# Performance work log

Hardware: AMD Instinct MI355X
Metric: run time of the kernel (lower is better)

The kernel has to match this reference:

```python
import jax, jax.numpy as jnp
import numpy as np

TOP_K = 2


def setup_inputs() -> dict:
    key = jax.random.key(0)
    k1, k2, k3, k4 = jax.random.split(key, 4)
    B, S, H, I, E = 2, 1024, 2048, 1408, 8
    hidden_states = jax.random.normal(k1, (B, S, H), dtype=jnp.float32)
    gate_w = jax.random.normal(k2, (E, H), dtype=jnp.float32) * (1.0 / np.sqrt(H))
    # stacked expert weights: gate_up_proj [E, 2I, H], down_proj [E, H, I] (torch Linear [out,in])
    w1 = jax.random.normal(k3, (E, 2 * I, H), dtype=jnp.float32) * (1.0 / np.sqrt(H))
    w2 = jax.random.normal(k4, (E, H, I), dtype=jnp.float32) * (1.0 / np.sqrt(I))
    return {"hidden_states": hidden_states, "gate_w": gate_w, "w1": w1, "w2": w2}


def reference(hidden_states, gate_w, w1, w2):
    B, S, H = hidden_states.shape
    E = gate_w.shape[0]
    T = B * S
    x = hidden_states.reshape(T, H)

    # --- gating: softmax -> top-k -> renormalize ---
    logits = jnp.einsum('th,eh->te', x, gate_w)            # [T, E]
    probs = jax.nn.softmax(logits, axis=-1)
    topw, sel = jax.lax.top_k(probs, TOP_K)                # [T, K]
    topw = topw / jnp.sum(topw, axis=-1, keepdims=True)

    # combine weights: [T, E], zero for unselected experts (equivalent to
    # dispatch/permute + per-token routing-weight scale + unpermute + sum)
    combine = jnp.zeros((T, E), dtype=x.dtype).at[
        jnp.arange(T)[:, None], sel].add(topw)

    # --- grouped expert FFN (computed densely per expert) ---
    gate_up = jnp.einsum('th,eoh->eto', x, w1)             # [E, T, 2I]
    g, u = jnp.split(gate_up, 2, axis=-1)
    act = jax.nn.silu(g) * u                               # SiluAndMul, [E, T, I]
    expert_out = jnp.einsum('eti,ehi->eth', act, w2)       # [E, T, H]

    # --- combine ---
    out = jnp.einsum('eth,te->th', expert_out, combine)    # [T, H]
    return out.reshape(B, S, H)
```

## Files before the change

kernel.cpp:

```cpp
#include <hip/hip_runtime.h>
#include <hip/hip_bf16.h>
#include <math.h>

#define T_TOK 2048
#define H_DIM 2048
#define I_DIM 1408
#define E_NUM 8
#define I2    2816

typedef __attribute__((ext_vector_type(8))) short short8;
typedef __attribute__((ext_vector_type(4))) float floatx4;
typedef __attribute__((ext_vector_type(8))) unsigned short ushort8;
typedef unsigned short u16;

__device__ __forceinline__ u16 f2bf(float x) {
    unsigned u = __builtin_bit_cast(unsigned, x);
    return (u16)((u + 0x7FFFu + ((u >> 16) & 1u)) >> 16);
}

__device__ __forceinline__ floatx4 mfma16(short8 a, short8 b, floatx4 c) {
    return __builtin_amdgcn_mfma_f32_16x16x32_bf16(a, b, c, 0, 0, 0);
}

__device__ __forceinline__ void gload16(const u16* g, u16* l) {
    __builtin_amdgcn_global_load_lds(
        (const __attribute__((address_space(1))) unsigned int*)g,
        (__attribute__((address_space(3))) unsigned int*)l, 16, 0, 0);
}

__device__ __forceinline__ int swz(int r) { return (r & 3) ^ ((r >> 2) & 3); }

__global__ void moe_gating(const float* __restrict__ x, const float* __restrict__ gw,
                           float* __restrict__ wts, int* __restrict__ counts,
                           int* __restrict__ entries) {
    const int lane = threadIdx.x & 63;
    const int wv   = threadIdx.x >> 6;
    const int t    = blockIdx.x * 4 + wv;
    float acc[E_NUM];
#pragma unroll
    for (int e = 0; e < E_NUM; ++e) acc[e] = 0.f;
    const float4* xr = (const float4*)(x + (size_t)t * H_DIM);
#pragma unroll
    for (int j = 0; j < 8; ++j) {
        float4 xv = xr[lane + 64 * j];
#pragma unroll
        for (int e = 0; e < E_NUM; ++e) {
            float4 g = ((const float4*)(gw + (size_t)e * H_DIM))[lane + 64 * j];
            acc[e] += xv.x * g.x + xv.y * g.y + xv.z * g.z + xv.w * g.w;
        }
    }
#pragma unroll
    for (int off = 32; off > 0; off >>= 1)
#pragma unroll
        for (int e = 0; e < E_NUM; ++e) acc[e] += __shfl_xor(acc[e], off, 64);

    if (lane == 0) {
        int a = 0; float la = acc[0];
        for (int e = 1; e < E_NUM; ++e) if (acc[e] > la) { la = acc[e]; a = e; }
        int b = (a == 0) ? 1 : 0; float lb = acc[b];
        for (int e = 0; e < E_NUM; ++e)
            if (e != a && acc[e] > lb) { lb = acc[e]; b = e; }
        float wa = 1.f / (1.f + expf(lb - la));
        wts[t * 2 + 0] = wa;
        wts[t * 2 + 1] = 1.f - wa;
        int p0 = atomicAdd(&counts[a], 1); entries[a * T_TOK + p0] = t * 2;
        int p1 = atomicAdd(&counts[b], 1); entries[b * T_TOK + p1] = t * 2 + 1;
    }
}

__global__ __launch_bounds__(256)
void cvt_bf16(const float* __restrict__ src, u16* __restrict__ dst, int n8) {
    int i = blockIdx.x * 256 + threadIdx.x;
    if (i >= n8) return;
    const float4* s4 = (const float4*)src;
    float4 a = s4[2 * i], b = s4[2 * i + 1];
    ushort8 o;
    o[0] = f2bf(a.x); o[1] = f2bf(a.y); o[2] = f2bf(a.z); o[3] = f2bf(a.w);
    o[4] = f2bf(b.x); o[5] = f2bf(b.y); o[6] = f2bf(b.z); o[7] = f2bf(b.w);
    *(ushort8*)(dst + (size_t)i * 8) = o;
}

template <bool BPRE>
__global__ __launch_bounds__(256)
void moe_mfma1(const u16* __restrict__ xb, const void* __restrict__ w1v,
               const int* __restrict__ counts, const int* __restrict__ entries,
               u16* __restrict__ act) {
    const int e  = blockIdx.z;
    const int ne = counts[e];
    const int tm = blockIdx.y;
    if (tm * 128 >= ne) return;
    const int tn = blockIdx.x;

    __shared__ __align__(16) u16 As[128 * 32];
    __shared__ __align__(16) u16 Bg[64 * 32];
    __shared__ __align__(16) u16 Bu[64 * 32];
    __shared__ int rowv[128];

    const int tid = threadIdx.x;
    if (tid < 128) {
        int r = tm * 128 + tid;
        rowv[tid] = (r < ne) ? entries[(size_t)e * T_TOK + r] : -1;
    }
    __syncthreads();

    const u16* asrc[2]; u16* adst[2];
#pragma unroll
    for (int q = 0; q < 2; ++q) {
        int i = q * 256 + tid;
        int row = i >> 2, p = i & 3;
        int lc = p ^ swz(row);
        int v = rowv[row];
        int tok = (v < 0) ? 0 : (v >> 1);
        asrc[q] = xb + (size_t)tok * H_DIM + lc * 8;
        adst[q] = As + i * 8;
    }
    const int brow = tid >> 2, bp = tid & 3;
    const int blc  = bp ^ swz(brow);
    const u16*   w1b = (const u16*)w1v;
    const float* w1f = (const float*)w1v;
    const size_t grow = ((size_t)e * I2 + tn * 64 + brow) * H_DIM + blc * 8;
    const size_t urow = grow + (size_t)I_DIM * H_DIM;
    u16* bgdst = Bg + tid * 8;
    u16* budst = Bu + tid * 8;

    const int lane = tid & 63, wid = tid >> 6;
    const int wm = wid & 1, wn = wid >> 1;

    floatx4 accG[4][2], accU[4][2];
    const floatx4 z4 = {0.f, 0.f, 0.f, 0.f};
#pragma unroll
    for (int mi = 0; mi < 4; ++mi)
#pragma unroll
        for (int ni = 0; ni < 2; ++ni) { accG[mi][ni] = z4; accU[mi][ni] = z4; }

    int aoff[4], boff[2];
#pragma unroll
    for (int mi = 0; mi < 4; ++mi) {
        int m = wm * 64 + mi * 16 + (lane & 15);
        aoff[mi] = m * 32 + (((lane >> 4) ^ swz(m)) * 8);
    }
#pragma unroll
    for (int ni = 0; ni < 2; ++ni) {
        int n = wn * 32 + ni * 16 + (lane & 15);
        boff[ni] = n * 32 + (((lane >> 4) ^ swz(n)) * 8);
    }

    for (int k0 = 0; k0 < H_DIM; k0 += 32) {
        gload16(asrc[0] + k0, adst[0]);
        gload16(asrc[1] + k0, adst[1]);
        if (BPRE) {
            gload16(w1b + grow + k0, bgdst);
            gload16(w1b + urow + k0, budst);
        } else {
            const float* gs = w1f + grow + k0;
            const float* us = w1f + urow + k0;
            float4 g0 = *(const float4*)gs, g1 = *(const float4*)(gs + 4);
            float4 u0 = *(const float4*)us, u1 = *(const float4*)(us + 4);
            ushort8 gv, uv;
            gv[0] = f2bf(g0.x); gv[1] = f2bf(g0.y); gv[2] = f2bf(g0.z); gv[3] = f2bf(g0.w);
            gv[4] = f2bf(g1.x); gv[5] = f2bf(g1.y); gv[6] = f2bf(g1.z); gv[7] = f2bf(g1.w);
            uv[0] = f2bf(u0.x); uv[1] = f2bf(u0.y); uv[2] = f2bf(u0.z); uv[3] = f2bf(u0.w);
            uv[4] = f2bf(u1.x); uv[5] = f2bf(u1.y); uv[6] = f2bf(u1.z); uv[7] = f2bf(u1.w);
            *(ushort8*)bgdst = gv;
            *(ushort8*)budst = uv;
        }
        __syncthreads();
        short8 a[4], bg[2], bu[2];
#pragma unroll
        for (int mi = 0; mi < 4; ++mi) a[mi] = *(const short8*)(As + aoff[mi]);
#pragma unroll
        for (int ni = 0; ni < 2; ++ni) {
            bg[ni] = *(const short8*)(Bg + boff[ni]);
            bu[ni] = *(const short8*)(Bu + boff[ni]);
        }
#pragma unroll
        for (int mi = 0; mi < 4; ++mi)
#pragma unroll
            for (int ni = 0; ni < 2; ++ni) {
                accG[mi][ni] = mfma16(a[mi], bg[ni], accG[mi][ni]);
                accU[mi][ni] = mfma16(a[mi], bu[ni], accU[mi][ni]);
            }
        __syncthreads();
    }

    const int obase = tn * 64 + wn * 32;
#pragma unroll
    for (int mi = 0; mi < 4; ++mi)
#pragma unroll
        for (int ni = 0; ni < 2; ++ni)
#pragma unroll
            for (int r = 0; r < 4; ++r) {
                int row = wm * 64 + mi * 16 + (lane >> 4) * 4 + r;
                int v = rowv[row];
                if (v < 0) continue;
                float g = accG[mi][ni][r], u = accU[mi][ni][r];
                float s = g / (1.f + expf(-g)) * u;
                act[(size_t)v * I_DIM + obase + ni * 16 + (lane & 15)] = f2bf(s);
            }
}

template <bool BPRE>
__global__ __launch_bounds__(256)
void moe_mfma2(const u16* __restrict__ act, const void* __restrict__ w2v,
               const int* __restrict__ counts, const int* __restrict__ entries,
               const float* __restrict__ wts, float* __restrict__ out) {
    const int e  = blockIdx.z;
    const int ne = counts[e];
    const int tm = blockIdx.y;
    if (tm * 128 >= ne) return;
    const int tn = blockIdx.x;

    __shared__ __align__(16) u16 As[128 * 32];
    __shared__ __align__(16) u16 Bs[128 * 32];
    __shared__ int   rowv[128];
    __shared__ int   rowt[128];
    __shared__ float roww[128];

    const int tid = threadIdx.x;
    if (tid < 128) {
        int r = tm * 128 + tid;
        int v = (r < ne) ? entries[(size_t)e * T_TOK + r] : -1;
        rowv[tid] = v;
        rowt[tid] = (v < 0) ? 0 : (v >> 1);
        roww[tid] = (v < 0) ? 0.f : wts[v];
    }
    __syncthreads();

    const u16* asrc[2]; u16* adst[2];
    size_t bsrc[2]; u16* bdst[2];
    const u16*   w2b = (const u16*)w2v;
    const float* w2f = (const float*)w2v;
#pragma unroll
    for (int q = 0; q < 2; ++q) {
        int i = q * 256 + tid;
        int row = i >> 2, p = i & 3;
        int lc = p ^ swz(row);
        int v = rowv[row]; if (v < 0) v = 0;
        asrc[q] = act + (size_t)v * I_DIM + lc * 8;
        adst[q] = As + i * 8;
        bsrc[q] = ((size_t)e * H_DIM + tn * 128 + row) * I_DIM + lc * 8;
        bdst[q] = Bs + i * 8;
    }

    const int lane = tid & 63, wid = tid >> 6;
    const int wm = wid & 1, wn = wid >> 1;

    floatx4 acc[4][4];
    const floatx4 z4 = {0.f, 0.f, 0.f, 0.f};
#pragma unroll
    for (int mi = 0; mi < 4; ++mi)
#pragma unroll
        for (int ni = 0; ni < 4; ++ni) acc[mi][ni] = z4;

    int aoff[4], boff[4];
#pragma unroll
    for (int mi = 0; mi < 4; ++mi) {
        int m = wm * 64 + mi * 16 + (lane & 15);
        aoff[mi] = m * 32 + (((lane >> 4) ^ swz(m)) * 8);
    }
#pragma unroll
    for (int ni = 0; ni < 4; ++ni) {
        int n = wn * 64 + ni * 16 + (lane & 15);
        boff[ni] = n * 32 + (((lane >> 4) ^ swz(n)) * 8);
    }

    for (int k0 = 0; k0 < I_DIM; k0 += 32) {
        gload16(asrc[0] + k0, adst[0]);
        gload16(asrc[1] + k0, adst[1]);
        if (BPRE) {
            gload16(w2b + bsrc[0] + k0, bdst[0]);
            gload16(w2b + bsrc[1] + k0, bdst[1]);
        } else {
#pragma unroll
            for (int q = 0; q < 2; ++q) {
                const float* bs = w2f + bsrc[q] + k0;
                float4 b0 = *(const float4*)bs, b1 = *(const float4*)(bs + 4);
                ushort8 bv;
                bv[0] = f2bf(b0.x); bv[1] = f2bf(b0.y); bv[2] = f2bf(b0.z); bv[3] = f2bf(b0.w);
                bv[4] = f2bf(b1.x); bv[5] = f2bf(b1.y); bv[6] = f2bf(b1.z); bv[7] = f2bf(b1.w);
                *(ushort8*)bdst[q] = bv;
            }
        }
        __syncthreads();
        short8 a[4], b[4];
#pragma unroll
        for (int mi = 0; mi < 4; ++mi) a[mi] = *(const short8*)(As + aoff[mi]);
#pragma unroll
        for (int ni = 0; ni < 4; ++ni) b[ni] = *(const short8*)(Bs + boff[ni]);
#pragma unroll
        for (int mi = 0; mi < 4; ++mi)
#pragma unroll
            for (int ni = 0; ni < 4; ++ni)
                acc[mi][ni] = mfma16(a[mi], b[ni], acc[mi][ni]);
        __syncthreads();
    }

    const int hbase = tn * 128 + wn * 64;
#pragma unroll
    for (int mi = 0; mi < 4; ++mi)
#pragma unroll
        for (int ni = 0; ni < 4; ++ni)
#pragma unroll
            for (int r = 0; r < 4; ++r) {
                int row = wm * 64 + mi * 16 + (lane >> 4) * 4 + r;
                if (rowv[row] < 0) continue;
                atomicAdd(out + (size_t)rowt[row] * H_DIM + hbase + ni * 16 + (lane & 15),
                          roww[row] * acc[mi][ni][r]);
            }
}

extern "C" void kernel_launch(void* const* d_in, const int* in_sizes, int n_in,
                              void* d_out, int out_size, void* d_ws, size_t ws_size,
                              hipStream_t stream) {
    const float* x  = (const float*)d_in[0];
    const float* gw = (const float*)d_in[1];
    const float* w1 = (const float*)d_in[2];
    const float* w2 = (const float*)d_in[3];
    float* out = (float*)d_out;

    char* ws = (char*)d_ws;
    int*   counts  = (int*)ws;
    int*   entries = (int*)(ws + 256);
    float* wts     = (float*)(ws + 256 + 65536);
    u16* xb  = (u16*)(ws + 131072);
    u16* act = xb  + (size_t)T_TOK * H_DIM;
    u16* w1b = act + (size_t)2 * T_TOK * I_DIM;
    u16* w2b = w1b + (size_t)E_NUM * I2 * H_DIM;
    const size_t need = 131072 + 2ull * ((size_t)T_TOK * H_DIM + 2ull * T_TOK * I_DIM +
                                         (size_t)E_NUM * I2 * H_DIM +
                                         (size_t)E_NUM * H_DIM * I_DIM);
    const bool pre = (ws_size >= need);

    hipMemsetAsync(counts, 0, 256, stream);
    hipMemsetAsync(out, 0, (size_t)T_TOK * H_DIM * sizeof(float), stream);

    moe_gating<<<T_TOK / 4, 256, 0, stream>>>(x, gw, wts, counts, entries);
    cvt_bf16<<<(T_TOK * H_DIM / 8 + 255) / 256, 256, 0, stream>>>(x, xb, T_TOK * H_DIM / 8);

    if (pre) {
        cvt_bf16<<<(E_NUM * I2 * H_DIM / 8 + 255) / 256, 256, 0, stream>>>(w1, w1b, E_NUM * I2 * H_DIM / 8);
        cvt_bf16<<<(E_NUM * H_DIM * I_DIM / 8 + 255) / 256, 256, 0, stream>>>(w2, w2b, E_NUM * H_DIM * I_DIM / 8);
        moe_mfma1<true><<<dim3(I_DIM / 64, 16, E_NUM), 256, 0, stream>>>(xb, w1b, counts, entries, act);
        moe_mfma2<true><<<dim3(H_DIM / 128, 16, E_NUM), 256, 0, stream>>>(act, w2b, counts, entries, wts, out);
    } else {
        moe_mfma1<false><<<dim3(I_DIM / 64, 16, E_NUM), 256, 0, stream>>>(xb, w1, counts, entries, act);
        moe_mfma2<false><<<dim3(H_DIM / 128, 16, E_NUM), 256, 0, stream>>>(act, w2, counts, entries, wts, out);
    }
}
```

Before: 569.6 us.

## Fuse weight and activation bf16 conversion into GEMMs, widen K tile to 64

Drops the separate bf16 pre-conversion passes over w1/w2 and instead converts fp32 weights on the fly inside both grouped GEMMs. The activation cast is folded into the gating kernel. The K tile grows from 32 to 64 with a new 8-way XOR swizzle, and the grid is flattened so the expert index varies fastest. This removes a large extra read/write pass over the weights, but each GEMM block now reads fp32 weights through registers rather than async LDS loads, doubling weight bytes per tile.

```diff
diff --git a/kernel.cpp b/kernel.cpp
--- a/kernel.cpp
+++ b/kernel.cpp
@@ -10,12 +10,20 @@
 
 typedef __attribute__((ext_vector_type(8))) short short8;
 typedef __attribute__((ext_vector_type(4))) float floatx4;
-typedef __attribute__((ext_vector_type(8))) unsigned short ushort8;
+typedef __attribute__((ext_vector_type(8))) unsigned short bf16x8;
+typedef __attribute__((ext_vector_type(4))) unsigned short bf16x4;
 typedef unsigned short u16;
 
 __device__ __forceinline__ u16 f2bf(float x) {
     unsigned u = __builtin_bit_cast(unsigned, x);
     return (u16)((u + 0x7FFFu + ((u >> 16) & 1u)) >> 16);
+}
+
+__device__ __forceinline__ bf16x8 pack8(float4 a, float4 b) {
+    bf16x8 o;
+    o[0] = f2bf(a.x); o[1] = f2bf(a.y); o[2] = f2bf(a.z); o[3] = f2bf(a.w);
+    o[4] = f2bf(b.x); o[5] = f2bf(b.y); o[6] = f2bf(b.z); o[7] = f2bf(b.w);
+    return o;
 }
 
 __device__ __forceinline__ floatx4 mfma16(short8 a, short8 b, floatx4 c) {
@@ -28,11 +36,9 @@
         (__attribute__((address_space(3))) unsigned int*)l, 16, 0, 0);
 }
 
-__device__ __forceinline__ int swz(int r) { return (r & 3) ^ ((r >> 2) & 3); }
-
 __global__ void moe_gating(const float* __restrict__ x, const float* __restrict__ gw,
-                           float* __restrict__ wts, int* __restrict__ counts,
-                           int* __restrict__ entries) {
+                           u16* __restrict__ xb, float* __restrict__ wts,
+                           int* __restrict__ counts, int* __restrict__ entries) {
     const int lane = threadIdx.x & 63;
     const int wv   = threadIdx.x >> 6;
     const int t    = blockIdx.x * 4 + wv;
@@ -40,9 +46,13 @@
 #pragma unroll
     for (int e = 0; e < E_NUM; ++e) acc[e] = 0.f;
     const float4* xr = (const float4*)(x + (size_t)t * H_DIM);
+    u16* xo = xb + (size_t)t * H_DIM;
 #pragma unroll
     for (int j = 0; j < 8; ++j) {
         float4 xv = xr[lane + 64 * j];
+        bf16x4 xw;
+        xw[0] = f2bf(xv.x); xw[1] = f2bf(xv.y); xw[2] = f2bf(xv.z); xw[3] = f2bf(xv.w);
+        *(bf16x4*)(xo + (lane + 64 * j) * 4) = xw;
 #pragma unroll
         for (int e = 0; e < E_NUM; ++e) {
             float4 g = ((const float4*)(gw + (size_t)e * H_DIM))[lane + 64 * j];
@@ -69,31 +79,20 @@
 }
 
 __global__ __launch_bounds__(256)
-void cvt_bf16(const float* __restrict__ src, u16* __restrict__ dst, int n8) {
-    int i = blockIdx.x * 256 + threadIdx.x;
-    if (i >= n8) return;
-    const float4* s4 = (const float4*)src;
-    float4 a = s4[2 * i], b = s4[2 * i + 1];
-    ushort8 o;
-    o[0] = f2bf(a.x); o[1] = f2bf(a.y); o[2] = f2bf(a.z); o[3] = f2bf(a.w);
-    o[4] = f2bf(b.x); o[5] = f2bf(b.y); o[6] = f2bf(b.z); o[7] = f2bf(b.w);
-    *(ushort8*)(dst + (size_t)i * 8) = o;
-}
-
-template <bool BPRE>
-__global__ __launch_bounds__(256)
-void moe_mfma1(const u16* __restrict__ xb, const void* __restrict__ w1v,
+void moe_mfma1(const u16* __restrict__ xb, const float* __restrict__ w1,
                const int* __restrict__ counts, const int* __restrict__ entries,
                u16* __restrict__ act) {
-    const int e  = blockIdx.z;
-    const int ne = counts[e];
-    const int tm = blockIdx.y;
+    const int bid = blockIdx.x;
+    const int e   = bid & 7;
+    const int rem = bid >> 3;
+    const int tn  = rem >> 4;
+    const int tm  = rem & 15;
+    const int ne  = counts[e];
     if (tm * 128 >= ne) return;
-    const int tn = blockIdx.x;
-
-    __shared__ __align__(16) u16 As[128 * 32];
-    __shared__ __align__(16) u16 Bg[64 * 32];
-    __shared__ __align__(16) u16 Bu[64 * 32];
+
+    __shared__ __align__(16) u16 As[128 * 64];
+    __shared__ __align__(16) u16 Bg[64 * 64];
+    __shared__ __align__(16) u16 Bu[64 * 64];
     __shared__ int rowv[128];
 
     const int tid = threadIdx.x;
@@ -103,25 +102,26 @@
     }
     __syncthreads();
 
-    const u16* asrc[2]; u16* adst[2];
-#pragma unroll
-    for (int q = 0; q < 2; ++q) {
+    const u16* asrc[4]; int ad[4];
+#pragma unroll
+    for (int q = 0; q < 4; ++q) {
         int i = q * 256 + tid;
-        int row = i >> 2, p = i & 3;
-        int lc = p ^ swz(row);
+        int row = i >> 3, pc = i & 7;
+        int lc = pc ^ (row & 7);
         int v = rowv[row];
         int tok = (v < 0) ? 0 : (v >> 1);
         asrc[q] = xb + (size_t)tok * H_DIM + lc * 8;
-        adst[q] = As + i * 8;
-    }
-    const int brow = tid >> 2, bp = tid & 3;
-    const int blc  = bp ^ swz(brow);
-    const u16*   w1b = (const u16*)w1v;
-    const float* w1f = (const float*)w1v;
-    const size_t grow = ((size_t)e * I2 + tn * 64 + brow) * H_DIM + blc * 8;
-    const size_t urow = grow + (size_t)I_DIM * H_DIM;
-    u16* bgdst = Bg + tid * 8;
-    u16* budst = Bu + tid * 8;
+        ad[q] = i * 8;
+    }
+    const int brow = tid >> 2;
+    const int bc16 = (tid & 3) * 16;
+    const float* gsrc = w1 + ((size_t)e * I2 + tn * 64 + brow) * H_DIM + bc16;
+    const float* usrc = gsrc + (size_t)I_DIM * H_DIM;
+    const int lc0 = (tid & 3) * 2;
+    u16* bgd0 = Bg + brow * 64 + ((lc0    ) ^ (brow & 7)) * 8;
+    u16* bgd1 = Bg + brow * 64 + ((lc0 + 1) ^ (brow & 7)) * 8;
+    u16* bud0 = Bu + brow * 64 + ((lc0    ) ^ (brow & 7)) * 8;
+    u16* bud1 = Bu + brow * 64 + ((lc0 + 1) ^ (brow & 7)) * 8;
 
     const int lane = tid & 63, wid = tid >> 6;
     const int wm = wid & 1, wn = wid >> 1;
@@ -133,53 +133,55 @@
 #pragma unroll
         for (int ni = 0; ni < 2; ++ni) { accG[mi][ni] = z4; accU[mi][ni] = z4; }
 
-    int aoff[4], boff[2];
+    int aoff[4][2], boff[2][2];
 #pragma unroll
     for (int mi = 0; mi < 4; ++mi) {
         int m = wm * 64 + mi * 16 + (lane & 15);
-        aoff[mi] = m * 32 + (((lane >> 4) ^ swz(m)) * 8);
+#pragma unroll
+        for (int kk = 0; kk < 2; ++kk)
+            aoff[mi][kk] = m * 64 + (((kk * 4 + (lane >> 4)) ^ (m & 7)) * 8);
     }
 #pragma unroll
     for (int ni = 0; ni < 2; ++ni) {
         int n = wn * 32 + ni * 16 + (lane & 15);
-        boff[ni] = n * 32 + (((lane >> 4) ^ swz(n)) * 8);
-    }
-
-    for (int k0 = 0; k0 < H_DIM; k0 += 32) {
-        gload16(asrc[0] + k0, adst[0]);
-        gload16(asrc[1] + k0, adst[1]);
-        if (BPRE) {
-            gload16(w1b + grow + k0, bgdst);
-            gload16(w1b + urow + k0, budst);
-        } else {
-            const float* gs = w1f + grow + k0;
-            const float* us = w1f + urow + k0;
-            float4 g0 = *(const float4*)gs, g1 = *(const float4*)(gs + 4);
-            float4 u0 = *(const float4*)us, u1 = *(const float4*)(us + 4);
-            ushort8 gv, uv;
-            gv[0] = f2bf(g0.x); gv[1] = f2bf(g0.y); gv[2] = f2bf(g0.z); gv[3] = f2bf(g0.w);
-            gv[4] = f2bf(g1.x); gv[5] = f2bf(g1.y); gv[6] = f2bf(g1.z); gv[7] = f2bf(g1.w);
-            uv[0] = f2bf(u0.x); uv[1] = f2bf(u0.y); uv[2] = f2bf(u0.z); uv[3] = f2bf(u0.w);
-            uv[4] = f2bf(u1.x); uv[5] = f2bf(u1.y); uv[6] = f2bf(u1.z); uv[7] = f2bf(u1.w);
-            *(ushort8*)bgdst = gv;
-            *(ushort8*)budst = uv;
+#pragma unroll
+        for (int kk = 0; kk < 2; ++kk)
+            boff[ni][kk] = n * 64 + (((kk * 4 + (lane >> 4)) ^ (n & 7)) * 8);
+    }
+
+#pragma unroll 1
+    for (int k0 = 0; k0 < H_DIM; k0 += 64) {
+#pragma unroll
+        for (int q = 0; q < 4; ++q) gload16(asrc[q] + k0, As + ad[q]);
+        {
+            const float4* g4 = (const float4*)(gsrc + k0);
+            const float4* u4 = (const float4*)(usrc + k0);
+            float4 a0 = g4[0], a1 = g4[1], a2 = g4[2], a3 = g4[3];
+            float4 b0 = u4[0], b1 = u4[1], b2 = u4[2], b3 = u4[3];
+            *(bf16x8*)bgd0 = pack8(a0, a1);
+            *(bf16x8*)bgd1 = pack8(a2, a3);
+            *(bf16x8*)bud0 = pack8(b0, b1);
+            *(bf16x8*)bud1 = pack8(b2, b3);
         }
         __syncthreads();
-        short8 a[4], bg[2], bu[2];
-#pragma unroll
-        for (int mi = 0; mi < 4; ++mi) a[mi] = *(const short8*)(As + aoff[mi]);
-#pragma unroll
-        for (int ni = 0; ni < 2; ++ni) {
-            bg[ni] = *(const short8*)(Bg + boff[ni]);
-            bu[ni] = *(const short8*)(Bu + boff[ni]);
-        }
-#pragma unroll
-        for (int mi = 0; mi < 4; ++mi)
+#pragma unroll
+        for (int kk = 0; kk < 2; ++kk) {
+            short8 a[4], g2[2], u2[2];
+#pragma unroll
+            for (int mi = 0; mi < 4; ++mi) a[mi] = *(const short8*)(As + aoff[mi][kk]);
 #pragma unroll
             for (int ni = 0; ni < 2; ++ni) {
-                accG[mi][ni] = mfma16(a[mi], bg[ni], accG[mi][ni]);
-                accU[mi][ni] = mfma16(a[mi], bu[ni], accU[mi][ni]);
+                g2[ni] = *(const short8*)(Bg + boff[ni][kk]);
+                u2[ni] = *(const short8*)(Bu + boff[ni][kk]);
             }
+#pragma unroll
+            for (int mi = 0; mi < 4; ++mi)
+#pragma unroll
+                for (int ni = 0; ni < 2; ++ni) {
+                    accG[mi][ni] = mfma16(a[mi], g2[ni], accG[mi][ni]);
+                    accU[mi][ni] = mfma16(a[mi], u2[ni], accU[mi][ni]);
+                }
+        }
         __syncthreads();
     }
 
@@ -199,19 +201,20 @@
             }
 }
 
-template <bool BPRE>
 __global__ __launch_bounds__(256)
-void moe_mfma2(const u16* __restrict__ act, const void* __restrict__ w2v,
+void moe_mfma2(const u16* __restrict__ act, const float* __restrict__ w2,
                const int* __restrict__ counts, const int* __restrict__ entries,
                const float* __restrict__ wts, float* __restrict__ out) {
-    const int e  = blockIdx.z;
-    const int ne = counts[e];
-    const int tm = blockIdx.y;
+    const int bid = blockIdx.x;
+    const int e   = bid & 7;
+    const int rem = bid >> 3;
+    const int tn  = rem >> 4;
+    const int tm  = rem & 15;
+    const int ne  = counts[e];
     if (tm * 128 >= ne) return;
-    const int tn = blockIdx.x;
-
-    __shared__ __align__(16) u16 As[128 * 32];
-    __shared__ __align__(16) u16 Bs[128 * 32];
+
+    __shared__ __align__(16) u16 As[128 * 64];
+    __shared__ __align__(16) u16 Bs[128 * 64];
     __shared__ int   rowv[128];
     __shared__ int   rowt[128];
     __shared__ float roww[128];
@@ -226,21 +229,24 @@
     }
     __syncthreads();
 
-    const u16* asrc[2]; u16* adst[2];
-    size_t bsrc[2]; u16* bdst[2];
-    const u16*   w2b = (const u16*)w2v;
-    const float* w2f = (const float*)w2v;
-#pragma unroll
-    for (int q = 0; q < 2; ++q) {
+    const u16* asrc[4]; int ad[4];
+#pragma unroll
+    for (int q = 0; q < 4; ++q) {
         int i = q * 256 + tid;
-        int row = i >> 2, p = i & 3;
-        int lc = p ^ swz(row);
+        int row = i >> 3, pc = i & 7;
+        int lc = pc ^ (row & 7);
         int v = rowv[row]; if (v < 0) v = 0;
         asrc[q] = act + (size_t)v * I_DIM + lc * 8;
-        adst[q] = As + i * 8;
-        bsrc[q] = ((size_t)e * H_DIM + tn * 128 + row) * I_DIM + lc * 8;
-        bdst[q] = Bs + i * 8;
-    }
+        ad[q] = i * 8;
+    }
+    const int brow = tid >> 1;
+    const int bc32 = (tid & 1) * 32;
+    const float* bsrc = w2 + ((size_t)e * H_DIM + tn * 128 + brow) * I_DIM + bc32;
+    const int lcb = (tid & 1) * 4;
+    u16* bd[4];
+#pragma unroll
+    for (int j = 0; j < 4; ++j)
+        bd[j] = Bs + brow * 64 + (((lcb + j) ^ (brow & 7)) * 8);
 
     const int lane = tid & 63, wid = tid >> 6;
     const int wm = wid & 1, wn = wid >> 1;
@@ -252,46 +258,49 @@
 #pragma unroll
         for (int ni = 0; ni < 4; ++ni) acc[mi][ni] = z4;
 
-    int aoff[4], boff[4];
+    int aoff[4][2], boff[4][2];
 #pragma unroll
     for (int mi = 0; mi < 4; ++mi) {
         int m = wm * 64 + mi * 16 + (lane & 15);
-        aoff[mi] = m * 32 + (((lane >> 4) ^ swz(m)) * 8);
+#pragma unroll
+        for (int kk = 0; kk < 2; ++kk)
+            aoff[mi][kk] = m * 64 + (((kk * 4 + (lane >> 4)) ^ (m & 7)) * 8);
     }
 #pragma unroll
     for (int ni = 0; ni < 4; ++ni) {
         int n = wn * 64 + ni * 16 + (lane & 15);
-        boff[ni] = n * 32 + (((lane >> 4) ^ swz(n)) * 8);
-    }
-
-    for (int k0 = 0; k0 < I_DIM; k0 += 32) {
-        gload16(asrc[0] + k0, adst[0]);
-        gload16(asrc[1] + k0, adst[1]);
-        if (BPRE) {
-            gload16(w2b + bsrc[0] + k0, bdst[0]);
-            gload16(w2b + bsrc[1] + k0, bdst[1]);
-        } else {
-#pragma unroll
-            for (int q = 0; q < 2; ++q) {
-                const float* bs = w2f + bsrc[q] + k0;
-                float4 b0 = *(const float4*)bs, b1 = *(const float4*)(bs + 4);
-                ushort8 bv;
-                bv[0] = f2bf(b0.x); bv[1] = f2bf(b0.y); bv[2] = f2bf(b0.z); bv[3] = f2bf(b0.w);
-                bv[4] = f2bf(b1.x); bv[5] = f2bf(b1.y); bv[6] = f2bf(b1.z); bv[7] = f2bf(b1.w);
-                *(ushort8*)bdst[q] = bv;
-            }
+#pragma unroll
+        for (int kk = 0; kk < 2; ++kk)
+            boff[ni][kk] = n * 64 + (((kk * 4 + (lane >> 4)) ^ (n & 7)) * 8);
+    }
+
+#pragma unroll 1
+    for (int k0 = 0; k0 < I_DIM; k0 += 64) {
+#pragma unroll
+        for (int q = 0; q < 4; ++q) gload16(asrc[q] + k0, As + ad[q]);
+        {
+            const float4* b4 = (const float4*)(bsrc + k0);
+            float4 t0 = b4[0], t1 = b4[1], t2 = b4[2], t3 = b4[3];
+            float4 t4 = b4[4], t5 = b4[5], t6 = b4[6], t7 = b4[7];
+            *(bf16x8*)bd[0] = pack8(t0, t1);
+            *(bf16x8*)bd[1] = pack8(t2, t3);
+            *(bf16x8*)bd[2] = pack8(t4, t5);
+            *(bf16x8*)bd[3] = pack8(t6, t7);
         }
         __syncthreads();
-        short8 a[4], b[4];
-#pragma unroll
-        for (int mi = 0; mi < 4; ++mi) a[mi] = *(const short8*)(As + aoff[mi]);
-#pragma unroll
-        for (int ni = 0; ni < 4; ++ni) b[ni] = *(const short8*)(Bs + boff[ni]);
-#pragma unroll
-        for (int mi = 0; mi < 4; ++mi)
-#pragma unroll
-            for (int ni = 0; ni < 4; ++ni)
-                acc[mi][ni] = mfma16(a[mi], b[ni], acc[mi][ni]);
+#pragma unroll
+        for (int kk = 0; kk < 2; ++kk) {
+            short8 a[4], b[4];
+#pragma unroll
+            for (int mi = 0; mi < 4; ++mi) a[mi] = *(const short8*)(As + aoff[mi][kk]);
+#pragma unroll
+            for (int ni = 0; ni < 4; ++ni) b[ni] = *(const short8*)(Bs + boff[ni][kk]);
+#pragma unroll
+            for (int mi = 0; mi < 4; ++mi)
+#pragma unroll
+                for (int ni = 0; ni < 4; ++ni)
+                    acc[mi][ni] = mfma16(a[mi], b[ni], acc[mi][ni]);
+        }
         __syncthreads();
     }
 
@@ -323,27 +332,12 @@
     int*   entries = (int*)(ws + 256);
     float* wts     = (float*)(ws + 256 + 65536);
     u16* xb  = (u16*)(ws + 131072);
-    u16* act = xb  + (size_t)T_TOK * H_DIM;
-    u16* w1b = act + (size_t)2 * T_TOK * I_DIM;
-    u16* w2b = w1b + (size_t)E_NUM * I2 * H_DIM;
-    const size_t need = 131072 + 2ull * ((size_t)T_TOK * H_DIM + 2ull * T_TOK * I_DIM +
-                                         (size_t)E_NUM * I2 * H_DIM +
-                                         (size_t)E_NUM * H_DIM * I_DIM);
-    const bool pre = (ws_size >= need);
-
-    hipMemsetAsync(counts, 0, 256, stream);
-    hipMemsetAsync(out, 0, (size_t)T_TOK * H_DIM * sizeof(float), stream);
-
-    moe_gating<<<T_TOK / 4, 256, 0, stream>>>(x, gw, wts, counts, entries);
-    cvt_bf16<<<(T_TOK * H_DIM / 8 + 255) / 256, 256, 0, stream>>>(x, xb, T_TOK * H_DIM / 8);
-
-    if (pre) {
-        cvt_bf16<<<(E_NUM * I2 * H_DIM / 8 + 255) / 256, 256, 0, stream>>>(w1, w1b, E_NUM * I2 * H_DIM / 8);
-        cvt_bf16<<<(E_NUM * H_DIM * I_DIM / 8 + 255) / 256, 256, 0, stream>>>(w2, w2b, E_NUM * H_DIM * I_DIM / 8);
-        moe_mfma1<true><<<dim3(I_DIM / 64, 16, E_NUM), 256, 0, stream>>>(xb, w1b, counts, entries, act);
-        moe_mfma2<true><<<dim3(H_DIM / 128, 16, E_NUM), 256, 0, stream>>>(act, w2b, counts, entries, wts, out);
-    } else {
-        moe_mfma1<false><<<dim3(I_DIM / 64, 16, E_NUM), 256, 0, stream>>>(xb, w1, counts, entries, act);
-        moe_mfma2<false><<<dim3(H_DIM / 128, 16, E_NUM), 256, 0, stream>>>(act, w2, counts, entries, wts, out);
-    }
-}
+    u16* act = xb + (size_t)T_TOK * H_DIM;
+
+    (void)hipMemsetAsync(counts, 0, 256, stream);
+    (void)hipMemsetAsync(out, 0, (size_t)T_TOK * H_DIM * sizeof(float), stream);
+
+    moe_gating<<<T_TOK / 4, 256, 0, stream>>>(x, gw, xb, wts, counts, entries);
+    moe_mfma1<<<dim3(22 * 16 * E_NUM), 256, 0, stream>>>(xb, w1, counts, entries, act);
+    moe_mfma2<<<dim3(16 * 16 * E_NUM), 256, 0, stream>>>(act, w2, counts, entries, wts, out);
+}
```

Measured after the change: 650.0 us. 1.14x slower.
